# Optimization experiments

Hardware: AMD Instinct MI355X
Metric: run time of the kernel (lower is better)

Reference implementation:

```python
import jax, jax.numpy as jnp
import numpy as np

NLAT, NLON = 256, 512
LMAX, MMAX = 256, 257  # legendre-gauss: lmax=nlat, mmax=nlon//2+1
BATCH, CHAN = 16, 8


def setup_inputs() -> dict:
    key = jax.random.key(0)
    kx, kw = jax.random.split(key)
    # vector field on the sphere: [..., 2 (theta/phi components), nlat, nlon]
    x = jax.random.normal(kx, (BATCH, CHAN, 2, NLAT, NLON), dtype=jnp.float32)
    # precomputed Legendre-derivative quadrature weights [2, mmax, lmax, nlat]
    # (stands in for precompute_dlegpoly * quad weights * 1/(l(l+1)), with weights[1] sign flip folded in)
    weights = 0.02 * jax.random.normal(kw, (2, MMAX, LMAX, NLAT), dtype=jnp.float32)
    return {"x": x, "weights": weights}


def reference(x, weights):
    # forward rfft over longitude, scaled by 2*pi (norm='forward' divides by nlon)
    xf = (2.0 * jnp.pi) * jnp.fft.rfft(x, axis=-1, norm="forward")  # [..., 2, nlat, nfreq] complex
    mmax = weights.shape[1]
    xf = xf[..., :mmax]
    # split vector components and real/imag parts
    xt = xf[..., 0, :, :]  # theta component [..., nlat, mmax]
    xp = xf[..., 1, :, :]  # phi component
    xtr, xti = jnp.real(xt), jnp.imag(xt)
    xpr, xpi = jnp.real(xp), jnp.imag(xp)
    w0 = weights[0]  # [mmax, lmax, nlat]
    w1 = weights[1]

    def contract(a, w):
        # batched per-m matmul: [..., k, m] x [m, l, k] -> [..., l, m]
        return jnp.einsum("...km,mlk->...lm", a, w)

    # spheroidal (component 0) and toroidal (component 1) coefficients
    out0 = (contract(xtr, w0) - contract(xpi, w1)) + 1j * (contract(xti, w0) + contract(xpr, w1))
    out1 = (-contract(xti, w1) - contract(xpr, w0)) + 1j * (contract(xtr, w1) - contract(xpi, w0))
    return jnp.stack([out0, out1], axis=-3)  # [..., 2, lmax, mmax] complex64
```

## Files before the change

kernel.cpp:

```cpp
#include <hip/hip_runtime.h>
#include <hip/hip_bf16.h>
#include <math.h>

#define NLAT 256
#define NLON 512
#define LMAX 256
#define MMAX 257
#define BC   128

#define X_ELEMS 33554432
#define W_ELEMS 33685504
#define W_BYTES (W_ELEMS * 4LL)

#define FM    288
#define F_BYTES  ((size_t)2*FM*512*2)
#define A_BYTES  ((size_t)4*BC*MMAX*NLAT*2)
#define OUTS_BYTES ((size_t)MMAX*2*BC*LMAX*2)

typedef short bf16x8 __attribute__((ext_vector_type(8)));
typedef float f32x4  __attribute__((ext_vector_type(4)));

__device__ __forceinline__ unsigned int bfpack2(float a, float b) {
    unsigned short lo = __builtin_bit_cast(unsigned short, __float2bfloat16(a));
    unsigned short hi = __builtin_bit_cast(unsigned short, __float2bfloat16(b));
    return (unsigned int)lo | ((unsigned int)hi << 16);
}
__device__ __forceinline__ unsigned short bf16bits(float a) {
    return __builtin_bit_cast(unsigned short, __float2bfloat16(a));
}
__device__ __forceinline__ void gload16(const void* g, void* l) {
    __builtin_amdgcn_global_load_lds(
        (const __attribute__((address_space(1))) unsigned int*)g,
        (__attribute__((address_space(3))) unsigned int*)l, 16, 0, 0);
}

__global__ __launch_bounds__(256) void f_init(unsigned short* __restrict__ F)
{
    int mm = blockIdx.x, o = blockIdx.y, t = threadIdx.x;
    const float s = 6.283185307179586f / 512.0f;
    for (int c = 0; c < 2; ++c) {
        int n = t * 2 + c;
        float val = 0.0f;
        if (mm < MMAX) {
            int j = (mm * n) & 511;
            float ang = 6.283185307179586f * (float)j / 512.0f;
            float sn, cs; __sincosf(ang, &sn, &cs);
            val = (o == 0) ? s * cs : -s * sn;
        }
        F[((size_t)o * FM + mm) * 512 + n] =
            __builtin_bit_cast(unsigned short, __float2bfloat16(val));
    }
}

__global__ __launch_bounds__(512, 1) void dft_mfma(const float* __restrict__ x,
                                                   const unsigned short* __restrict__ F,
                                                   unsigned short* __restrict__ aout)
{
    __shared__ __align__(16) unsigned char fl[2][32768];
    unsigned char* xl = (unsigned char*)fl;

    int bcc = blockIdx.x;
    int kh  = blockIdx.y;
    int bc = bcc >> 1, comp = bcc & 1;
    int t = threadIdx.x;
    int wid = t >> 6, lane = t & 63;

    int o = wid >> 2, kt = wid & 3;
    int r15 = lane & 15, hi = lane >> 4;
    int klocal = kt * 16 + r15;
    unsigned braw = (unsigned)klocal * 1024u;
    unsigned bswz = (unsigned)(klocal & 15) << 4;

    bf16x8 barr0[16], barr1[16];
    #pragma unroll
    for (int s = 0; s < 2; ++s) {
        const float* xg = x + ((size_t)bcc * NLAT + kh * 128 + s * 64) * NLON;
        #pragma unroll
        for (int p = 0; p < 8; ++p) {
            int row = wid * 8 + p;
            const float* src = xg + (size_t)row * NLON + lane * 8;
            float4 f0 = *(const float4*)(src);
            float4 f1 = *(const float4*)(src + 4);
            uint4 v;
            v.x = bfpack2(f0.x, f0.y); v.y = bfpack2(f0.z, f0.w);
            v.z = bfpack2(f1.x, f1.y); v.w = bfpack2(f1.z, f1.w);
            unsigned off = ((unsigned)row * 1024u + (unsigned)lane * 16u)
                           ^ ((unsigned)(row & 15) << 4);
            *(uint4*)(xl + off) = v;
        }
        __syncthreads();
        #pragma unroll
        for (int nt = 0; nt < 16; ++nt) {
            unsigned c0 = (unsigned)(nt * 64 + hi * 16);
            bf16x8 v = *(const bf16x8*)(xl + ((braw + c0) ^ bswz));
            if (s == 0) barr0[nt] = v; else barr1[nt] = v;
        }
        __syncthreads();
    }

    const unsigned char* Fb = (const unsigned char*)F;
    unsigned gcol = ((unsigned)lane * 16u);

    #define STAGE_F(buf, mt)                                                  \
        {                                                                     \
            _Pragma("unroll")                                                 \
            for (int p = 0; p < 4; ++p) {                                     \
                int fr = wid * 4 + p;                                         \
                int o2 = fr >> 4, mr = fr & 15;                               \
                size_t grow = (size_t)o2 * FM + (mt) * 16 + mr;               \
                const void* g = Fb + grow * 1024u                             \
                                + (gcol ^ ((unsigned)(fr & 15) << 4));        \
                gload16(g, (unsigned char*)fl[buf] + (unsigned)fr * 1024u);   \
            }                                                                 \
        }

    STAGE_F(0, 0);
    __syncthreads();

    unsigned arow = (unsigned)(o * 16 + r15);
    unsigned abase = arow * 1024u;
    unsigned aswz = (unsigned)r15 << 4;
    unsigned short* ao = aout;
    int v = comp * 2 + o;

    for (int mt = 0; mt < 17; ++mt) {
        int cur = mt & 1;
        if (mt < 16) STAGE_F(cur ^ 1, mt + 1);

        const unsigned char* fb = fl[cur];
        f32x4 accA0 = {0.f,0.f,0.f,0.f}, accA1 = {0.f,0.f,0.f,0.f};
        f32x4 accB0 = {0.f,0.f,0.f,0.f}, accB1 = {0.f,0.f,0.f,0.f};
        #pragma unroll
        for (int nt = 0; nt < 16; nt += 2) {
            unsigned c0 = (unsigned)(nt * 64 + hi * 16);
            bf16x8 a0 = *(const bf16x8*)(fb + ((abase + c0)       ^ aswz));
            bf16x8 a1 = *(const bf16x8*)(fb + ((abase + c0 + 64u) ^ aswz));
            accA0 = __builtin_amdgcn_mfma_f32_16x16x32_bf16(a0, barr0[nt],     accA0, 0, 0, 0);
            accB0 = __builtin_amdgcn_mfma_f32_16x16x32_bf16(a0, barr1[nt],     accB0, 0, 0, 0);
            accA1 = __builtin_amdgcn_mfma_f32_16x16x32_bf16(a1, barr0[nt + 1], accA1, 0, 0, 0);
            accB1 = __builtin_amdgcn_mfma_f32_16x16x32_bf16(a1, barr1[nt + 1], accB1, 0, 0, 0);
        }
        #pragma unroll
        for (int j = 0; j < 4; ++j) {
            accA0[j] += accA1[j];
            accB0[j] += accB1[j];
        }

        #pragma unroll
        for (int j = 0; j < 4; ++j) {
            int mm0 = mt * 16 + hi * 4 + j;
            if (mm0 < MMAX) {
                size_t base = (((size_t)v * BC + bc) * MMAX + mm0) * NLAT + kh * 128;
                ao[base + klocal]      = bf16bits(accA0[j]);
                ao[base + klocal + 64] = bf16bits(accB0[j]);
            }
        }
        __syncthreads();
    }
    #undef STAGE_F
}

template <int MODE>
__global__ __launch_bounds__(512, 1) void contract_mfma(const unsigned short* __restrict__ a,
                                                        const float* __restrict__ w,
                                                        void* __restrict__ outv)
{
    __shared__ __align__(16) unsigned char Ab[2][16384];
    __shared__ __align__(16) unsigned char Bb[2][10240];
    int m  = blockIdx.x;
    int lh = blockIdx.y;
    int t = threadIdx.x;
    int wid = t >> 6, lane = t & 63;
    int o = wid >> 2, h = (wid >> 1) & 1, q = wid & 1;
    int r15 = lane & 15, hi = lane >> 4;
    int l0 = lh * 128;

    f32x4 accLo[4][4] = {};
    f32x4 accHi[4][4] = {};

    int bcr = t >> 2, ch4 = t & 3;
    int lB  = t >> 2, chB = t & 3;

    #define STAGE_A(buf, kt)                                                    \
        {                                                                       \
            int ph_ = (kt) >> 3;                                                \
            int k0_ = ((kt) & 7) * 32;                                          \
            _Pragma("unroll")                                                   \
            for (int i = 0; i < 2; ++i) {                                       \
                int vsel = (i == 0) ? (ph_ ? 3 : 0) : (ph_ ? 1 : 2);            \
                const void* g = a + (((size_t)vsel * BC + bcr) * MMAX + m) * NLAT \
                                  + k0_ + (ch4 ^ (bcr & 3)) * 8;                \
                gload16(g, Ab[buf] + wid * 1024 + i * 8192);                    \
            }                                                                   \
        }

    float4 wreg0, wreg1;
    #define WLOAD(kt)                                                           \
        {                                                                       \
            int ph_ = (kt) >> 3;                                                \
            int k0_ = ((kt) & 7) * 32;                                          \
            const float* wp = w + (((size_t)ph_ * MMAX + m) * LMAX + l0 + lB) * NLAT \
                                + k0_ + chB * 8;                                \
            wreg0 = *(const float4*)(wp);                                       \
            wreg1 = *(const float4*)(wp + 4);                                   \
        }
    #define BWRITE(buf)                                                         \
        {                                                                       \
            uint4 vv;                                                           \
            vv.x = bfpack2(wreg0.x, wreg0.y); vv.y = bfpack2(wreg0.z, wreg0.w); \
            vv.z = bfpack2(wreg1.x, wreg1.y); vv.w = bfpack2(wreg1.z, wreg1.w); \
            *(uint4*)(Bb[buf] + lB * 80 + chB * 16) = vv;                       \
        }
    #define MFMA_PHASE(ACC)                                                     \
        {                                                                       \
            bf16x8 bfr[4];                                                      \
            _Pragma("unroll")                                                   \
            for (int lt = 0; lt < 4; ++lt)                                      \
                bfr[lt] = *(const bf16x8*)(bb + (q * 64 + lt * 16 + r15) * 80 + hi * 16); \
            _Pragma("unroll")                                                   \
            for (int bt = 0; bt < 4; ++bt) {                                    \
                bf16x8 af = *(const bf16x8*)(ab + (o * 128 + h * 64 + bt * 16 + r15) * 64 \
                                               + ((hi * 16) ^ ((r15 & 3) << 4))); \
                _Pragma("unroll")                                               \
                for (int lt = 0; lt < 4; ++lt)                                  \
                    ACC[bt][lt] = __builtin_amdgcn_mfma_f32_16x16x32_bf16(af, bfr[lt], ACC[bt][lt], 0, 0, 0); \
            }                                                                   \
        }

    STAGE_A(0, 0);
    WLOAD(0);
    __syncthreads();
    BWRITE(0);

    for (int kt2 = 0; kt2 < 16; ++kt2) {
        int cur = kt2 & 1;
        if (kt2 < 15) WLOAD(kt2 + 1);
        __syncthreads();
        if (kt2 < 15) STAGE_A(cur ^ 1, kt2 + 1);

        const unsigned char* bb = Bb[cur];
        const unsigned char* ab = Ab[cur];
        if (kt2 < 8) MFMA_PHASE(accLo) else MFMA_PHASE(accHi);

        if (kt2 < 15) BWRITE(cur ^ 1);
    }

    #pragma unroll
    for (int bt = 0; bt < 4; ++bt) {
        #pragma unroll
        for (int lt = 0; lt < 4; ++lt) {
            #pragma unroll
            for (int j = 0; j < 4; ++j) {
                int bc = h * 64 + bt * 16 + hi * 4 + j;
                int l  = l0 + q * 64 + lt * 16 + r15;
                float lo = accLo[bt][lt][j];
                float hh = accHi[bt][lt][j];
                float val = (o == 0) ? (lo - hh) : (0.0f - (lo + hh));
                if (MODE == 0) {
                    __hip_bfloat16* outs = (__hip_bfloat16*)outv;
                    outs[(((size_t)m * 2 + o) * BC + bc) * LMAX + l] = __float2bfloat16(val);
                } else {
                    float* out = (float*)outv;
                    out[(((size_t)bc * 2 + o) * LMAX + l) * MMAX + m] = val;
                }
            }
        }
    }
    #undef STAGE_A
    #undef WLOAD
    #undef BWRITE
    #undef MFMA_PHASE
}

__global__ __launch_bounds__(256) void transpose_out(const unsigned short* __restrict__ outs,
                                                     float* __restrict__ out)
{
    __shared__ float tile[32][65];
    int mt = blockIdx.x;
    int lt = blockIdx.y;
    int z  = blockIdx.z;
    int bc = z >> 1, o = z & 1;
    int t = threadIdx.x;

    {
        int r = t >> 3, c0 = (t & 7) * 8;
        int mm = mt * 32 + r;
        if (mm < MMAX) {
            const unsigned short* src = outs + (((size_t)mm * 2 + o) * BC + bc) * LMAX + lt * 64 + c0;
            uint4 v = *(const uint4*)src;
            const unsigned short* u = (const unsigned short*)&v;
            #pragma unroll
            for (int i = 0; i < 8; ++i)
                tile[r][c0 + i] = __bfloat162float(__builtin_bit_cast(__hip_bfloat16, u[i]));
        }
    }
    __syncthreads();
    {
        int l = t >> 2, mc = (t & 3) * 8;
        float* dst = out + (((size_t)bc * 2 + o) * LMAX + lt * 64 + l) * MMAX + mt * 32 + mc;
        #pragma unroll
        for (int i = 0; i < 8; ++i) {
            int mm = mt * 32 + mc + i;
            if (mm < MMAX) dst[i] = tile[mc + i][l];
        }
    }
}

#define PER_BC ((size_t)4 * MMAX * NLAT * sizeof(__hip_bfloat16))

__global__ __launch_bounds__(256) void dft_legacy(const float* __restrict__ x,
                                                  __hip_bfloat16* __restrict__ a,
                                                  int bc0, int nbc)
{
    __shared__ float  xs[512];
    __shared__ float2 tw[512];
    int t = threadIdx.x;
    int b = blockIdx.x;
    int lat = b & (NLAT - 1);
    int comp = (b >> 8) & 1;
    int bcl = b >> 9;
    int bc = bc0 + bcl;
    const float* xr = x + (((size_t)bc * 2 + comp) * NLAT + lat) * NLON;
    for (int j = t; j < 512; j += 256) {
        xs[j] = xr[j];
        float ang = -6.283185307179586f * (float)j / 512.0f;
        float sn, cs; sincosf(ang, &sn, &cs);
        tw[j] = make_float2(cs, sn);
    }
    __syncthreads();
    const float scale = 6.283185307179586f / 512.0f;
    size_t VS = (size_t)nbc * MMAX * NLAT;
    __hip_bfloat16* p0 = a + (size_t)(comp * 2) * VS + (size_t)bcl * MMAX * NLAT + lat;
    __hip_bfloat16* p1 = p0 + VS;
    for (int m = t; m < MMAX; m += 256) {
        float accr = 0.f, acci = 0.f;
        int j = 0;
        for (int n = 0; n < 512; ++n) {
            float xv = xs[n]; float2 wv = tw[j];
            accr += xv * wv.x; acci += xv * wv.y;
            j = (j + m) & 511;
        }
        p0[(size_t)m * NLAT] = __float2bfloat16(accr * scale);
        p1[(size_t)m * NLAT] = __float2bfloat16(acci * scale);
    }
}

__global__ __launch_bounds__(256) void contract_legacy(const __hip_bfloat16* __restrict__ a,
                                                       const float* __restrict__ w,
                                                       float* __restrict__ out,
                                                       int bc0, int nbc)
{
    __shared__ float w0s[16][NLAT + 1];
    __shared__ float w1s[16][NLAT + 1];
    __shared__ float as[4][4][NLAT + 1];
    __shared__ float2 red2[256];
    int tid = threadIdx.x;
    int m = blockIdx.x, l0 = blockIdx.y * 16, bct = blockIdx.z * 4;
    const float* w0g = w + ((size_t)m * LMAX + l0) * NLAT;
    const float* w1g = w0g + (size_t)MMAX * LMAX * NLAT;
    for (int idx = tid; idx < 16 * NLAT; idx += 256) {
        int l = idx >> 8, k = idx & 255;
        w0s[l][k] = w0g[(size_t)l * NLAT + k];
        w1s[l][k] = w1g[(size_t)l * NLAT + k];
    }
    size_t VS = (size_t)nbc * MMAX * NLAT;
    for (int idx = tid; idx < 4 * 4 * NLAT; idx += 256) {
        int v = idx >> 10, bl = (idx >> 8) & 3, k = idx & 255;
        int bls = bct + bl; if (bls > nbc - 1) bls = nbc - 1;
        as[v][bl][k] = __bfloat162float(a[(size_t)v * VS + ((size_t)bls * MMAX + m) * NLAT + k]);
    }
    __syncthreads();
    int l = tid & 15, b = (tid >> 4) & 3, kseg = tid >> 6;
    float acc0 = 0.f, acc2 = 0.f;
    int kbeg = kseg * 64;
    #pragma unroll 8
    for (int k = kbeg; k < kbeg + 64; ++k) {
        float tr = as[0][b][k], ti = as[1][b][k], pr = as[2][b][k], pi = as[3][b][k];
        float w0 = w0s[l][k], w1 = w1s[l][k];
        acc0 += tr * w0 - pi * w1;
        acc2 -= ti * w1 + pr * w0;
    }
    red2[tid] = make_float2(acc0, acc2);
    __syncthreads();
    if (kseg == 0 && (bct + b) < nbc) {
        #pragma unroll
        for (int s = 1; s < 4; ++s) {
            float2 r = red2[tid + 64 * s];
            acc0 += r.x; acc2 += r.y;
        }
        int bc = bc0 + bct + b;
        out[(((size_t)bc * 2 + 0) * LMAX + (l0 + l)) * MMAX + m] = acc0;
        out[(((size_t)bc * 2 + 1) * LMAX + (l0 + l)) * MMAX + m] = acc2;
    }
}

extern "C" void kernel_launch(void* const* d_in, const int* in_sizes, int n_in,
                              void* d_out, int out_size, void* d_ws, size_t ws_size,
                              hipStream_t stream)
{
    const float* x = (const float*)d_in[0];
    const float* w = (const float*)d_in[1];
    if (n_in >= 2) {
        long long s0 = (long long)in_sizes[0];
        if (s0 == (long long)W_ELEMS || s0 == W_BYTES) {
            w = (const float*)d_in[0];
            x = (const float*)d_in[1];
        }
    }
    float* out = (float*)d_out;

    if (ws_size >= F_BYTES + A_BYTES) {
        unsigned short* F = (unsigned short*)d_ws;
        unsigned short* a = (unsigned short*)((char*)d_ws + F_BYTES);
        hipLaunchKernelGGL(f_init, dim3(FM, 2), dim3(256), 0, stream, F);
        hipLaunchKernelGGL(dft_mfma, dim3(256, 2), dim3(512), 0, stream, x, F, a);
        if (ws_size >= F_BYTES + A_BYTES + OUTS_BYTES) {
            unsigned short* outs = (unsigned short*)((char*)d_ws + F_BYTES + A_BYTES);
            hipLaunchKernelGGL((contract_mfma<0>), dim3(MMAX, 2), dim3(512), 0, stream,
                               a, w, (void*)outs);
            hipLaunchKernelGGL(transpose_out, dim3(9, 4, 256), dim3(256), 0, stream,
                               outs, out);
        } else {
            hipLaunchKernelGGL((contract_mfma<1>), dim3(MMAX, 2), dim3(512), 0, stream,
                               a, w, (void*)out);
        }
    } else {
        __hip_bfloat16* a = (__hip_bfloat16*)d_ws;
        int nbc = 1;
        for (int c = 128; c >= 1; c >>= 1)
            if (PER_BC * (size_t)c <= ws_size) { nbc = c; break; }
        int nchunks = BC / nbc;
        for (int cc = 0; cc < nchunks; ++cc) {
            int bc0 = cc * nbc;
            hipLaunchKernelGGL(dft_legacy, dim3(nbc * 2 * NLAT), dim3(256), 0, stream,
                               x, a, bc0, nbc);
            hipLaunchKernelGGL(contract_legacy, dim3(MMAX, LMAX / 16, (nbc + 3) / 4),
                               dim3(256), 0, stream, a, w, out, bc0, nbc);
        }
    }
}
```

Measured before the change: 206.4 us.

## Merge l-halves into one 1024-thread block per m with pre-negated weight tile

The contraction kernel now launches one 1024-thread block per m covering all 256 l rows, instead of two 512-thread blocks that each loaded the same A tiles. The weight tile is staged twice in shared memory, once as is and once with the bf16 sign bit flipped, so that the subtraction for output 0 folds into the accumulation. This lets each wave keep a single accumulator set instead of separate low and high phase sets. The cost is more shared memory (about 114 KB), fewer and larger blocks with one block per CU, and extra LDS stores for the negated copy.

```diff
diff --git a/kernel.cpp b/kernel.cpp
--- a/kernel.cpp
+++ b/kernel.cpp
@@ -161,37 +161,34 @@
 }
 
 template <int MODE>
-__global__ __launch_bounds__(512, 1) void contract_mfma(const unsigned short* __restrict__ a,
-                                                        const float* __restrict__ w,
-                                                        void* __restrict__ outv)
+__global__ __launch_bounds__(1024, 1) void contract_mfma(const unsigned short* __restrict__ a,
+                                                         const float* __restrict__ w,
+                                                         void* __restrict__ outv)
 {
     __shared__ __align__(16) unsigned char Ab[2][16384];
-    __shared__ __align__(16) unsigned char Bb[2][10240];
+    __shared__ __align__(16) unsigned char Bb[2][40960];
     int m  = blockIdx.x;
-    int lh = blockIdx.y;
     int t = threadIdx.x;
     int wid = t >> 6, lane = t & 63;
-    int o = wid >> 2, h = (wid >> 1) & 1, q = wid & 1;
+    int o = wid >> 3, h = (wid >> 2) & 1, q = wid & 3;
     int r15 = lane & 15, hi = lane >> 4;
-    int l0 = lh * 128;
-
-    f32x4 accLo[4][4] = {};
-    f32x4 accHi[4][4] = {};
-
-    int bcr = t >> 2, ch4 = t & 3;
-    int lB  = t >> 2, chB = t & 3;
+
+    f32x4 acc[4][4] = {};
+
+    int pl  = t >> 9;
+    int bcr = (t >> 2) & 127;
+    int ch4 = t & 3;
+    int lB  = t >> 2;
+    int chB = t & 3;
 
     #define STAGE_A(buf, kt)                                                    \
         {                                                                       \
             int ph_ = (kt) >> 3;                                                \
             int k0_ = ((kt) & 7) * 32;                                          \
-            _Pragma("unroll")                                                   \
-            for (int i = 0; i < 2; ++i) {                                       \
-                int vsel = (i == 0) ? (ph_ ? 3 : 0) : (ph_ ? 1 : 2);            \
-                const void* g = a + (((size_t)vsel * BC + bcr) * MMAX + m) * NLAT \
-                                  + k0_ + (ch4 ^ (bcr & 3)) * 8;                \
-                gload16(g, Ab[buf] + wid * 1024 + i * 8192);                    \
-            }                                                                   \
+            int vsel = (pl == 0) ? (ph_ ? 3 : 0) : (ph_ ? 1 : 2);               \
+            const void* g = a + (((size_t)vsel * BC + bcr) * MMAX + m) * NLAT   \
+                              + k0_ + (ch4 ^ (bcr & 3)) * 8;                    \
+            gload16(g, Ab[buf] + wid * 1024);                                   \
         }
 
     float4 wreg0, wreg1;
@@ -199,7 +196,7 @@
         {                                                                       \
             int ph_ = (kt) >> 3;                                                \
             int k0_ = ((kt) & 7) * 32;                                          \
-            const float* wp = w + (((size_t)ph_ * MMAX + m) * LMAX + l0 + lB) * NLAT \
+            const float* wp = w + (((size_t)ph_ * MMAX + m) * LMAX + lB) * NLAT \
                                 + k0_ + chB * 8;                                \
             wreg0 = *(const float4*)(wp);                                       \
             wreg1 = *(const float4*)(wp + 4);                                   \
@@ -210,21 +207,10 @@
             vv.x = bfpack2(wreg0.x, wreg0.y); vv.y = bfpack2(wreg0.z, wreg0.w); \
             vv.z = bfpack2(wreg1.x, wreg1.y); vv.w = bfpack2(wreg1.z, wreg1.w); \
             *(uint4*)(Bb[buf] + lB * 80 + chB * 16) = vv;                       \
-        }
-    #define MFMA_PHASE(ACC)                                                     \
-        {                                                                       \
-            bf16x8 bfr[4];                                                      \
-            _Pragma("unroll")                                                   \
-            for (int lt = 0; lt < 4; ++lt)                                      \
-                bfr[lt] = *(const bf16x8*)(bb + (q * 64 + lt * 16 + r15) * 80 + hi * 16); \
-            _Pragma("unroll")                                                   \
-            for (int bt = 0; bt < 4; ++bt) {                                    \
-                bf16x8 af = *(const bf16x8*)(ab + (o * 128 + h * 64 + bt * 16 + r15) * 64 \
-                                               + ((hi * 16) ^ ((r15 & 3) << 4))); \
-                _Pragma("unroll")                                               \
-                for (int lt = 0; lt < 4; ++lt)                                  \
-                    ACC[bt][lt] = __builtin_amdgcn_mfma_f32_16x16x32_bf16(af, bfr[lt], ACC[bt][lt], 0, 0, 0); \
-            }                                                                   \
+            uint4 vn;                                                           \
+            vn.x = vv.x ^ 0x80008000u; vn.y = vv.y ^ 0x80008000u;               \
+            vn.z = vv.z ^ 0x80008000u; vn.w = vv.w ^ 0x80008000u;               \
+            *(uint4*)(Bb[buf] + 20480 + lB * 80 + chB * 16) = vn;               \
         }
 
     STAGE_A(0, 0);
@@ -238,9 +224,20 @@
         __syncthreads();
         if (kt2 < 15) STAGE_A(cur ^ 1, kt2 + 1);
 
-        const unsigned char* bb = Bb[cur];
+        const unsigned char* bb = Bb[cur] + ((o == 0 && kt2 >= 8) ? 20480 : 0);
         const unsigned char* ab = Ab[cur];
-        if (kt2 < 8) MFMA_PHASE(accLo) else MFMA_PHASE(accHi);
+        bf16x8 bfr[4];
+        #pragma unroll
+        for (int lt = 0; lt < 4; ++lt)
+            bfr[lt] = *(const bf16x8*)(bb + (q * 64 + lt * 16 + r15) * 80 + hi * 16);
+        #pragma unroll
+        for (int bt = 0; bt < 4; ++bt) {
+            bf16x8 af = *(const bf16x8*)(ab + (o * 128 + h * 64 + bt * 16 + r15) * 64
+                                           + ((hi * 16) ^ ((r15 & 3) << 4)));
+            #pragma unroll
+            for (int lt = 0; lt < 4; ++lt)
+                acc[bt][lt] = __builtin_amdgcn_mfma_f32_16x16x32_bf16(af, bfr[lt], acc[bt][lt], 0, 0, 0);
+        }
 
         if (kt2 < 15) BWRITE(cur ^ 1);
     }
@@ -252,10 +249,9 @@
             #pragma unroll
             for (int j = 0; j < 4; ++j) {
                 int bc = h * 64 + bt * 16 + hi * 4 + j;
-                int l  = l0 + q * 64 + lt * 16 + r15;
-                float lo = accLo[bt][lt][j];
-                float hh = accHi[bt][lt][j];
-                float val = (o == 0) ? (lo - hh) : (0.0f - (lo + hh));
+                int l  = q * 64 + lt * 16 + r15;
+                float av = acc[bt][lt][j];
+                float val = (o == 0) ? av : (0.0f - av);
                 if (MODE == 0) {
                     __hip_bfloat16* outs = (__hip_bfloat16*)outv;
                     outs[(((size_t)m * 2 + o) * BC + bc) * LMAX + l] = __float2bfloat16(val);
@@ -269,7 +265,6 @@
     #undef STAGE_A
     #undef WLOAD
     #undef BWRITE
-    #undef MFMA_PHASE
 }
 
 __global__ __launch_bounds__(256) void transpose_out(const unsigned short* __restrict__ outs,
@@ -416,12 +411,12 @@
         hipLaunchKernelGGL(dft_mfma, dim3(256, 2), dim3(512), 0, stream, x, F, a);
         if (ws_size >= F_BYTES + A_BYTES + OUTS_BYTES) {
             unsigned short* outs = (unsigned short*)((char*)d_ws + F_BYTES + A_BYTES);
-            hipLaunchKernelGGL((contract_mfma<0>), dim3(MMAX, 2), dim3(512), 0, stream,
+            hipLaunchKernelGGL((contract_mfma<0>), dim3(MMAX), dim3(1024), 0, stream,
                                a, w, (void*)outs);
             hipLaunchKernelGGL(transpose_out, dim3(9, 4, 256), dim3(256), 0, stream,
                                outs, out);
         } else {
-            hipLaunchKernelGGL((contract_mfma<1>), dim3(MMAX, 2), dim3(512), 0, stream,
+            hipLaunchKernelGGL((contract_mfma<1>), dim3(MMAX), dim3(1024), 0, stream,
                                a, w, (void*)out);
         }
     } else {
```

Result: no change. 206.7 us (+0.2%).
